# Optimization experiments

Hardware: AMD Instinct MI355X
Metric: run time of the kernel (lower is better)

The kernel has to match this reference:

```python
import jax, jax.numpy as jnp
import numpy as np

B, LQ, LK, DIM = 2, 2048, 2048, 1024
HEADS, DH = 8, 64
INNER = HEADS * DH  # 512


def setup_inputs() -> dict:
    key = jax.random.key(0)
    ks = jax.random.split(key, 7)
    x = jax.random.normal(ks[0], (B, LQ, DIM), dtype=jnp.float32)
    y = jax.random.normal(ks[1], (B, LK, DIM), dtype=jnp.float32)
    # binary mask, 1 => masked (gets -1e9 added)
    mask = jax.random.randint(ks[2], (B, LQ, LK), 0, 2).astype(jnp.float32)
    s = 0.02
    Wq = jax.random.normal(ks[3], (INNER, DIM), dtype=jnp.float32) * s
    Wk = jax.random.normal(ks[4], (INNER, DIM), dtype=jnp.float32) * s
    Wv = jax.random.normal(ks[5], (INNER, DIM), dtype=jnp.float32) * s
    Wo = jax.random.normal(ks[6], (DIM, INNER), dtype=jnp.float32) * s
    return {"x": x, "y": y, "mask": mask, "Wq": Wq, "Wk": Wk, "Wv": Wv, "Wo": Wo}


def reference(x, y, mask, Wq, Wk, Wv, Wo):
    scale = DH ** -0.5
    # projections (Linear without bias: x @ W.T)
    q = (x @ Wq.T) * scale            # [B, LQ, INNER]
    k = y @ Wk.T                      # [B, LK, INNER]
    v = y @ Wv.T                      # [B, LK, INNER]
    # split into heads (torch.split along last dim == reshape to [.., H, DH])
    q = q.reshape(B, LQ, HEADS, DH)
    k = k.reshape(B, LK, HEADS, DH)
    v = v.reshape(B, LK, HEADS, DH)
    # per-head QK^T + additive mask*-1e9, softmax over keys, then V
    scores = jnp.einsum('bqhd,bkhd->bhqk', q, k) + mask[:, None, :, :] * (-1e9)
    attn = jax.nn.softmax(scores, axis=-1)
    out = jnp.einsum('bhqk,bkhd->bqhd', attn, v).reshape(B, LQ, INNER)
    return out @ Wo.T                 # [B, LQ, DIM]
```

## Files before the change

### kernel.cpp

```cpp
#include <hip/hip_runtime.h>
#include <hip/hip_bf16.h>
#include <stdint.h>

#define BATCH 2
#define LQ 2048
#define LK 2048
#define DIM 1024
#define HEADS 8
#define DH 64
#define INNER 512

typedef __attribute__((ext_vector_type(8))) short short8;
typedef __attribute__((ext_vector_type(4))) float f32x4;

__device__ __forceinline__ float bf2f(unsigned short u) {
    union { unsigned int i; float f; } v;
    v.i = ((unsigned int)u) << 16;
    return v.f;
}
__device__ __forceinline__ unsigned short f2bf(float f) {
    __hip_bfloat16 h = __float2bfloat16(f);
    return *reinterpret_cast<unsigned short*>(&h);
}
__device__ __forceinline__ float fexp2(float x) {
#if __has_builtin(__builtin_amdgcn_exp2f)
    return __builtin_amdgcn_exp2f(x);
#else
    return __expf(x * 0.69314718056f);
#endif
}
__device__ __forceinline__ void stc(unsigned short* C, size_t i, float v) { C[i] = f2bf(v); }
__device__ __forceinline__ void stc(float* C, size_t i, float v) { C[i] = v; }

__device__ __forceinline__ unsigned cvtpk_bf16(float lo, float hi) {
    unsigned r;
    asm("v_cvt_pk_bf16_f32 %0, %1, %2" : "=v"(r) : "v"(lo), "v"(hi));
    return r;
}
__device__ __forceinline__ void perm32swap(unsigned& a, unsigned& b) {
#if __has_builtin(__builtin_amdgcn_permlane32_swap)
    auto r = __builtin_amdgcn_permlane32_swap(a, b, false, false);
    a = r[0]; b = r[1];
#else
    asm volatile("v_permlane32_swap_b32 %0, %1" : "+v"(a), "+v"(b));
#endif
}
__device__ __forceinline__ void perm16swap(unsigned& a, unsigned& b) {
#if __has_builtin(__builtin_amdgcn_permlane16_swap)
    auto r = __builtin_amdgcn_permlane16_swap(a, b, false, false);
    a = r[0]; b = r[1];
#else
    asm volatile("v_permlane16_swap_b32 %0, %1" : "+v"(a), "+v"(b));
#endif
}

typedef __attribute__((address_space(1))) const unsigned int gu32;
typedef __attribute__((address_space(3))) unsigned int lu32;
__device__ __forceinline__ void gload16(const void* g, void* l) {
    __builtin_amdgcn_global_load_lds((gu32*)g, (lu32*)l, 16, 0, 0);
}

__global__ __launch_bounds__(256) void prep(
    const float* __restrict__ x,  const float* __restrict__ y,
    const float* __restrict__ wq, const float* __restrict__ wk,
    const float* __restrict__ wv, const float* __restrict__ wo,
    const float* __restrict__ mask,
    unsigned short* __restrict__ xb,  unsigned short* __restrict__ yb,
    unsigned short* __restrict__ wqb, unsigned short* __restrict__ wkb,
    unsigned short* __restrict__ wvb, unsigned short* __restrict__ wob,
    unsigned long long* __restrict__ mbits)
{
    if (blockIdx.y == 6) {
        const int wid = blockIdx.x * 4 + (threadIdx.x >> 6);
        const int lane = threadIdx.x & 63;
        for (int task = wid; task < BATCH * LQ * 8; task += 4096) {
            int row = task >> 3, g = task & 7;
            const float* mp = mask + (size_t)row * LK + g * 256;
            unsigned long long* ob = mbits + (size_t)row * (LK / 64) + g * 4;
            float v0 = mp[0 * 64 + lane];
            float v1 = mp[1 * 64 + lane];
            float v2 = mp[2 * 64 + lane];
            float v3 = mp[3 * 64 + lane];
            unsigned long long b0 = __ballot(v0 > 0.5f);
            unsigned long long b1 = __ballot(v1 > 0.5f);
            unsigned long long b2 = __ballot(v2 > 0.5f);
            unsigned long long b3 = __ballot(v3 > 0.5f);
            if (lane == 0) { ob[0] = b0; ob[1] = b1; ob[2] = b2; ob[3] = b3; }
        }
        return;
    }
    const float* src; unsigned short* dst; int n4;
    switch (blockIdx.y) {
        case 0: src = x;  dst = xb;  n4 = (BATCH * LQ * DIM) / 4; break;
        case 1: src = y;  dst = yb;  n4 = (BATCH * LK * DIM) / 4; break;
        case 2: src = wq; dst = wqb; n4 = (INNER * DIM) / 4; break;
        case 3: src = wk; dst = wkb; n4 = (INNER * DIM) / 4; break;
        case 4: src = wv; dst = wvb; n4 = (INNER * DIM) / 4; break;
        default: src = wo; dst = wob; n4 = (INNER * DIM) / 4; break;
    }
    const int stride = gridDim.x * 256;
    for (int i = blockIdx.x * 256 + threadIdx.x; i < n4; i += stride) {
        float4 f = ((const float4*)src)[i];
        ushort4 u;
        u.x = f2bf(f.x); u.y = f2bf(f.y); u.z = f2bf(f.z); u.w = f2bf(f.w);
        ((ushort4*)dst)[i] = u;
    }
}

template <int IM, int JN, int WR, int WC, typename TC, int EPI>
__device__ __forceinline__ void gemm_body(
    const unsigned short* __restrict__ A,
    const unsigned short* __restrict__ W,
    TC* __restrict__ C,
    int K, int N, float scale,
    unsigned short* SH)
{
    constexpr int THREADS = WR * WC * 64;
    constexpr int BM = WR * IM * 16;
    constexpr int BN = WC * JN * 16;
    constexpr int ACH = BM * 8;
    constexpr int BCH = BN * 8;
    constexpr int AUS = BM * 64;
    constexpr int BUS = BN * 64;

    unsigned short* As = SH;
    unsigned short* Bs = SH + 2 * AUS;

    const int tid = threadIdx.x;
    const int m0 = blockIdx.x * BM;
    const int n0 = blockIdx.y * BN;
    const int w = tid >> 6, lane = tid & 63;
    const int q4 = lane >> 4, l16 = lane & 15;
    const int wm = (w / WC) * (IM * 16), wn = (w % WC) * (JN * 16);
    const int sw = l16 & 7;

    f32x4 acc[IM][JN] = {};

#pragma unroll
    for (int i = 0; i < ACH / THREADS; ++i) {
        int s = tid + i * THREADS;
        int r = s >> 3, ch = (s & 7) ^ (r & 7);
        gload16(A + (size_t)(m0 + r) * K + ch * 8, As + (size_t)s * 8);
    }
#pragma unroll
    for (int i = 0; i < BCH / THREADS; ++i) {
        int s = tid + i * THREADS;
        int r = s >> 3, ch = (s & 7) ^ (r & 7);
        gload16(W + (size_t)(n0 + r) * K + ch * 8, Bs + (size_t)s * 8);
    }
    __syncthreads();

    const int nt = K / 64;
    for (int t = 0; t < nt; ++t) {
        const int curA = (t & 1) * AUS;
        const int curB = (t & 1) * BUS;
        if (t + 1 < nt) {
            int kk = (t + 1) * 64;
            const int nxtA = AUS - curA, nxtB = BUS - curB;
#pragma unroll
            for (int i = 0; i < ACH / THREADS; ++i) {
                int s = tid + i * THREADS;
                int r = s >> 3, ch = (s & 7) ^ (r & 7);
                gload16(A + (size_t)(m0 + r) * K + kk + ch * 8, As + nxtA + (size_t)s * 8);
            }
#pragma unroll
            for (int i = 0; i < BCH / THREADS; ++i) {
                int s = tid + i * THREADS;
                int r = s >> 3, ch = (s & 7) ^ (r & 7);
                gload16(W + (size_t)(n0 + r) * K + kk + ch * 8, Bs + nxtB + (size_t)s * 8);
            }
        }

#pragma unroll
        for (int ks = 0; ks < 2; ++ks) {
            const int kq = ((ks * 4 + q4) ^ sw) * 8;
            short8 a[IM], b[JN];
#pragma unroll
            for (int i = 0; i < IM; ++i)
                a[i] = *(const short8*)(As + curA + (wm + i * 16 + l16) * 64 + kq);
#pragma unroll
            for (int j = 0; j < JN; ++j)
                b[j] = *(const short8*)(Bs + curB + (wn + j * 16 + l16) * 64 + kq);
#pragma unroll
            for (int i = 0; i < IM; ++i)
#pragma unroll
                for (int j = 0; j < JN; ++j)
                    acc[i][j] = __builtin_amdgcn_mfma_f32_16x16x32_bf16(
                        a[i], b[j], acc[i][j], 0, 0, 0);
        }
        __syncthreads();
    }

    if (EPI == 0) {
#pragma unroll
        for (int i = 0; i < IM; ++i)
#pragma unroll
            for (int j = 0; j < JN; ++j)
#pragma unroll
                for (int r = 0; r < 4; ++r) {
                    int row = m0 + wm + i * 16 + q4 * 4 + r;
                    int col = n0 + wn + j * 16 + l16;
                    stc(C, (size_t)row * N + col, acc[i][j][r] * scale);
                }
    } else {
        constexpr int KW = IM * 16;
        constexpr int DW = JN * 16;
        constexpr int TPS = KW + 8;
        unsigned short* TP = SH + w * (DW * TPS);
#pragma unroll
        for (int i = 0; i < IM; ++i)
#pragma unroll
            for (int j = 0; j < JN; ++j) {
                ushort4 u;
                u.x = f2bf(acc[i][j][0]); u.y = f2bf(acc[i][j][1]);
                u.z = f2bf(acc[i][j][2]); u.w = f2bf(acc[i][j][3]);
                *(ushort4*)(TP + (j * 16 + l16) * TPS + i * 16 + q4 * 4) = u;
            }
        const int keyflat = m0 + wm;
        const int bb = keyflat >> 11, key0 = keyflat & (LK - 1);
        const int hh = (n0 + wn) >> 6;
        const int dlow = (n0 + wn) & 63;
        constexpr int RCH = KW / 8;
        constexpr int NCH = DW * RCH;
#pragma unroll
        for (int p = 0; p < NCH / 64; ++p) {
            int c = p * 64 + lane;
            int dl = c / RCH, kc = c % RCH;
            uint4 v = *(const uint4*)(TP + dl * TPS + kc * 8);
            *(uint4*)((unsigned short*)C +
                ((size_t)((bb * HEADS + hh) * DH + dlow + dl)) * LK + key0 + kc * 8) = v;
        }
    }
}

#define QSCALE 0.18033688011112042f

__global__ __launch_bounds__(512) void proj_qkv(
    const unsigned short* __restrict__ xb, const unsigned short* __restrict__ yb,
    const unsigned short* __restrict__ wqb, const unsigned short* __restrict__ wkb,
    const unsigned short* __restrict__ wvb,
    unsigned short* __restrict__ qb, unsigned short* __restrict__ kb,
    unsigned short* __restrict__ vt)
{
    __shared__ __align__(16) unsigned short SH[4 * 128 * 64];
    const int z = blockIdx.z;
    const unsigned short* A = (z == 0) ? xb : yb;
    const unsigned short* W = (z == 0) ? wqb : (z == 1) ? wkb : wvb;
    if (z == 2)
        gemm_body<4, 2, 2, 4, unsigned short, 1>(A, W, vt, DIM, INNER, 1.0f, SH);
    else
        gemm_body<4, 2, 2, 4, unsigned short, 0>(A, W, (z == 0) ? qb : kb, DIM, INNER,
                                                 (z == 0) ? QSCALE : 1.0f, SH);
}

__global__ __launch_bounds__(512) void gemm_out(
    const unsigned short* __restrict__ A,
    const unsigned short* __restrict__ W,
    float* __restrict__ C)
{
    __shared__ __align__(16) unsigned short SH[4 * 128 * 64];
    gemm_body<4, 2, 2, 4, float, 0>(A, W, C, INNER, DIM, 1.0f, SH);
}

#define AT_SLOT (64 * 64)

__global__ __launch_bounds__(512, 4) void attn_mfma(
    const unsigned short* __restrict__ Q,
    const unsigned short* __restrict__ Kb,
    const unsigned short* __restrict__ Vt,
    const unsigned long long* __restrict__ Mb,
    unsigned short* __restrict__ O)
{
    __shared__ __align__(16) unsigned short Ks[4 * AT_SLOT];
    __shared__ __align__(16) unsigned short Vs[4 * AT_SLOT];

    const int tid = threadIdx.x;
    const int L = blockIdx.x;
    const int h = L & 7;
    const int jj = L >> 3;
    const int b = jj >> 5;
    const int q0 = (jj & 31) * 64;
    const int w = tid >> 6, lane = tid & 63;
    const int g = w & 3;
    const int par = w >> 2;
    const int q4 = lane >> 4, l16 = lane & 15;
    const int sw = l16 & 7;

    short8 qf[2];
    {
        const unsigned short* qp =
            Q + (size_t)(b * LQ + q0 + g * 16 + l16) * INNER + h * DH + q4 * 8;
        qf[0] = *(const short8*)(qp);
        qf[1] = *(const short8*)(qp + 32);
    }

    f32x4 o[4] = {};
    float lacc = 0.f;

    const unsigned short* kbase = Kb + (size_t)(b * LK) * INNER + h * DH;
    const unsigned short* vbase = Vt + (size_t)((b * HEADS + h) * DH) * LK;
    const unsigned long long* mrow =
        Mb + (size_t)(b * LQ + q0 + g * 16 + l16) * (LK / 64);

    const int rr = tid >> 3;
    const int ch = (tid & 7) ^ (rr & 7);

#pragma unroll
    for (int tn = 0; tn < 2; ++tn) {
        gload16(kbase + (size_t)(tn * 64 + rr) * INNER + ch * 8,
                Ks + tn * AT_SLOT + (size_t)tid * 8);
        gload16(vbase + (size_t)rr * LK + tn * 64 + ch * 8,
                Vs + tn * AT_SLOT + (size_t)tid * 8);
    }
    __syncthreads();

    const int NR = LK / 128;
    for (int rd = 0; rd < NR; ++rd) {
        if (rd + 1 < NR) {
#pragma unroll
            for (int i = 0; i < 2; ++i) {
                const int tn = 2 * rd + 2 + i;
                const int sl = tn & 3;
                gload16(kbase + (size_t)(tn * 64 + rr) * INNER + ch * 8,
                        Ks + sl * AT_SLOT + (size_t)tid * 8);
                gload16(vbase + (size_t)rr * LK + tn * 64 + ch * 8,
                        Vs + sl * AT_SLOT + (size_t)tid * 8);
            }
        }
        const int t = 2 * rd + par;
        const int cur = (t & 3) * AT_SLOT;

        f32x4 s[4];
        __builtin_amdgcn_s_setprio(1);
#pragma unroll
        for (int j = 0; j < 4; ++j) {
            s[j] = f32x4{0.f, 0.f, 0.f, 0.f};
#pragma unroll
            for (int ks = 0; ks < 2; ++ks) {
                short8 kf = *(const short8*)(Ks + cur + (j * 16 + l16) * 64
                                             + (((ks * 4 + q4) ^ sw) * 8));
                s[j] = __builtin_amdgcn_mfma_f32_16x16x32_bf16(kf, qf[ks], s[j], 0, 0, 0);
            }
        }
        __builtin_amdgcn_s_setprio(0);

        unsigned long long bsh = mrow[t] >> (q4 * 4);
        unsigned pk[8];
#pragma unroll
        for (int j = 0; j < 4; ++j) {
            unsigned nib = (unsigned)(bsh >> (16 * j)) & 0xFu;
            float p0 = (nib & 1u) ? 0.f : fexp2(s[j][0]);
            float p1 = (nib & 2u) ? 0.f : fexp2(s[j][1]);
            float p2 = (nib & 4u) ? 0.f : fexp2(s[j][2]);
            float p3 = (nib & 8u) ? 0.f : fexp2(s[j][3]);
            lacc += (p0 + p1) + (p2 + p3);
            pk[2 * j]     = cvtpk_bf16(p0, p1);
            pk[2 * j + 1] = cvtpk_bf16(p2, p3);
        }

        short8 pf[2];
#pragma unroll
        for (int ks = 0; ks < 2; ++ks) {
            unsigned a0 = pk[4 * ks + 0], b0 = pk[4 * ks + 2];
            unsigned a1 = pk[4 * ks + 1], b1 = pk[4 * ks + 3];
            perm32swap(a0, b0); perm16swap(a0, b0);
            perm32swap(a1, b1); perm16swap(a1, b1);
            union { unsigned u[4]; short8 s8; } up;
            up.u[0] = a0; up.u[1] = a1; up.u[2] = b0; up.u[3] = b1;
            pf[ks] = up.s8;
        }

        __builtin_amdgcn_s_setprio(1);
#pragma unroll
        for (int ks = 0; ks < 2; ++ks) {
#pragma unroll
            for (int dd = 0; dd < 4; ++dd) {
                short8 vf = *(const short8*)(Vs + cur + (dd * 16 + l16) * 64
                                             + (((ks * 4 + q4) ^ sw) * 8));
                o[dd] = __builtin_amdgcn_mfma_f32_16x16x32_bf16(vf, pf[ks], o[dd], 0, 0, 0);
            }
        }
        __builtin_amdgcn_s_setprio(0);
        __syncthreads();
    }

    float* xch = (float*)Ks;
    if (par) {
        float* d = xch + (size_t)(g * 64 + lane) * 17;
#pragma unroll
        for (int dd = 0; dd < 4; ++dd)
#pragma unroll
            for (int r2 = 0; r2 < 4; ++r2) d[dd * 4 + r2] = o[dd][r2];
        d[16] = lacc;
    }
    __syncthreads();
    if (!par) {
        const float* d = xch + (size_t)(g * 64 + lane) * 17;
#pragma unroll
        for (int dd = 0; dd < 4; ++dd)
#pragma unroll
            for (int r2 = 0; r2 < 4; ++r2) o[dd][r2] += d[dd * 4 + r2];
        lacc += d[16];

        lacc += __shfl_xor(lacc, 16);
        lacc += __shfl_xor(lacc, 32);
        const float inv = 1.0f / lacc;

        unsigned short* orow =
            O + (size_t)(b * LQ + q0 + g * 16 + l16) * INNER + h * DH + q4 * 4;
#pragma unroll
        for (int dd = 0; dd < 4; ++dd) {
            ushort4 u;
            u.x = f2bf(o[dd][0] * inv); u.y = f2bf(o[dd][1] * inv);
            u.z = f2bf(o[dd][2] * inv); u.w = f2bf(o[dd][3] * inv);
            *(ushort4*)(orow + dd * 16) = u;
        }
    }
}

extern "C" void kernel_launch(void* const* d_in, const int* in_sizes, int n_in,
                              void* d_out, int out_size, void* d_ws, size_t ws_size,
                              hipStream_t stream) {
    const float* x    = (const float*)d_in[0];
    const float* y    = (const float*)d_in[1];
    const float* mask = (const float*)d_in[2];
    const float* Wq   = (const float*)d_in[3];
    const float* Wk   = (const float*)d_in[4];
    const float* Wv   = (const float*)d_in[5];
    const float* Wo   = (const float*)d_in[6];
    float* out = (float*)d_out;

    const size_t NX = (size_t)BATCH * LQ * DIM;
    const size_t NS = (size_t)BATCH * LQ * INNER;
    const size_t NW = (size_t)INNER * DIM;
    unsigned short* xb  = (unsigned short*)d_ws;
    unsigned short* yb  = xb + NX;
    unsigned short* qb  = yb + NX;
    unsigned short* kb  = qb + NS;
    unsigned short* vt  = kb + NS;
    unsigned short* wqb = vt + NS;
    unsigned short* wkb = wqb + NW;
    unsigned short* wvb = wkb + NW;
    unsigned short* wob = wvb + NW;
    unsigned long long* mbits = (unsigned long long*)(wob + NW);
    unsigned short* ao  = xb;

    dim3 blk(256);
    prep<<<dim3(1024, 7), blk, 0, stream>>>(
        x, y, Wq, Wk, Wv, Wo, mask, xb, yb, wqb, wkb, wvb, wob, mbits);
    proj_qkv<<<dim3(4096 / 128, INNER / 128, 3), dim3(512), 0, stream>>>(
        xb, yb, wqb, wkb, wvb, qb, kb, vt);
    attn_mfma<<<dim3(512), dim3(512), 0, stream>>>(
        qb, kb, vt, mbits, ao);
    gemm_out<<<dim3(4096 / 128, DIM / 128), dim3(512), 0, stream>>>(ao, wob, out);
}
```

Baseline: 174.0 us.

## Switch attention kernel to 32x32x16 MFMA tiles with four-way wave reduction

Rewrites the attention inner loop to use 32x32x16 bf16 MFMA instructions instead of 16x16x32. Each wave now covers 32 query rows and half of a 64-key tile, which reduces the number of MFMA issues and LDS fragment loads per tile. The P-matrix repack needs only permlane32 swaps. In exchange, partial outputs are split four ways across waves and must be reduced through LDS at the end, and the larger accumulators raise register pressure.

```diff
diff --git a/kernel.cpp b/kernel.cpp
--- a/kernel.cpp
+++ b/kernel.cpp
@@ -12,6 +12,7 @@
 
 typedef __attribute__((ext_vector_type(8))) short short8;
 typedef __attribute__((ext_vector_type(4))) float f32x4;
+typedef __attribute__((ext_vector_type(16))) float f32x16;
 
 __device__ __forceinline__ float bf2f(unsigned short u) {
     union { unsigned int i; float f; } v;
@@ -43,14 +44,6 @@
     a = r[0]; b = r[1];
 #else
     asm volatile("v_permlane32_swap_b32 %0, %1" : "+v"(a), "+v"(b));
-#endif
-}
-__device__ __forceinline__ void perm16swap(unsigned& a, unsigned& b) {
-#if __has_builtin(__builtin_amdgcn_permlane16_swap)
-    auto r = __builtin_amdgcn_permlane16_swap(a, b, false, false);
-    a = r[0]; b = r[1];
-#else
-    asm volatile("v_permlane16_swap_b32 %0, %1" : "+v"(a), "+v"(b));
 #endif
 }
 
@@ -281,26 +274,27 @@
     const int b = jj >> 5;
     const int q0 = (jj & 31) * 64;
     const int w = tid >> 6, lane = tid & 63;
-    const int g = w & 3;
+    const int qh = w & 1;
+    const int kh = (w >> 1) & 1;
     const int par = w >> 2;
-    const int q4 = lane >> 4, l16 = lane & 15;
-    const int sw = l16 & 7;
-
-    short8 qf[2];
+    const int l31 = lane & 31, hl = lane >> 5;
+
+    short8 qf[4];
     {
         const unsigned short* qp =
-            Q + (size_t)(b * LQ + q0 + g * 16 + l16) * INNER + h * DH + q4 * 8;
-        qf[0] = *(const short8*)(qp);
-        qf[1] = *(const short8*)(qp + 32);
-    }
-
-    f32x4 o[4] = {};
+            Q + (size_t)(b * LQ + q0 + qh * 32 + l31) * INNER + h * DH + 8 * hl;
+#pragma unroll
+        for (int ks = 0; ks < 4; ++ks)
+            qf[ks] = *(const short8*)(qp + ks * 16);
+    }
+
+    f32x16 o[2] = {};
     float lacc = 0.f;
 
     const unsigned short* kbase = Kb + (size_t)(b * LK) * INNER + h * DH;
     const unsigned short* vbase = Vt + (size_t)((b * HEADS + h) * DH) * LK;
     const unsigned long long* mrow =
-        Mb + (size_t)(b * LQ + q0 + g * 16 + l16) * (LK / 64);
+        Mb + (size_t)(b * LQ + q0 + qh * 32 + l31) * (LK / 64);
 
     const int rr = tid >> 3;
     const int ch = (tid & 7) ^ (rr & 7);
@@ -314,6 +308,7 @@
     }
     __syncthreads();
 
+    const int l7 = lane & 7;
     const int NR = LK / 128;
     for (int rd = 0; rd < NR; ++rd) {
         if (rd + 1 < NR) {
@@ -330,91 +325,95 @@
         const int t = 2 * rd + par;
         const int cur = (t & 3) * AT_SLOT;
 
-        f32x4 s[4];
+        f32x16 s = {};
         __builtin_amdgcn_s_setprio(1);
 #pragma unroll
-        for (int j = 0; j < 4; ++j) {
-            s[j] = f32x4{0.f, 0.f, 0.f, 0.f};
-#pragma unroll
-            for (int ks = 0; ks < 2; ++ks) {
-                short8 kf = *(const short8*)(Ks + cur + (j * 16 + l16) * 64
-                                             + (((ks * 4 + q4) ^ sw) * 8));
-                s[j] = __builtin_amdgcn_mfma_f32_16x16x32_bf16(kf, qf[ks], s[j], 0, 0, 0);
-            }
+        for (int ks = 0; ks < 4; ++ks) {
+            const int R = kh * 32 + l31;
+            const int c0 = ks * 2 + hl;
+            short8 kf = *(const short8*)(Ks + cur + R * 64 + ((c0 ^ l7) * 8));
+            s = __builtin_amdgcn_mfma_f32_32x32x16_bf16(kf, qf[ks], s, 0, 0, 0);
         }
         __builtin_amdgcn_s_setprio(0);
 
-        unsigned long long bsh = mrow[t] >> (q4 * 4);
+        unsigned bits32 = (unsigned)(mrow[t] >> (kh * 32));
         unsigned pk[8];
 #pragma unroll
-        for (int j = 0; j < 4; ++j) {
-            unsigned nib = (unsigned)(bsh >> (16 * j)) & 0xFu;
-            float p0 = (nib & 1u) ? 0.f : fexp2(s[j][0]);
-            float p1 = (nib & 2u) ? 0.f : fexp2(s[j][1]);
-            float p2 = (nib & 4u) ? 0.f : fexp2(s[j][2]);
-            float p3 = (nib & 8u) ? 0.f : fexp2(s[j][3]);
+        for (int g = 0; g < 4; ++g) {
+            unsigned nib = (bits32 >> (8 * g + 4 * hl)) & 0xFu;
+            float p0 = (nib & 1u) ? 0.f : fexp2(s[4 * g + 0]);
+            float p1 = (nib & 2u) ? 0.f : fexp2(s[4 * g + 1]);
+            float p2 = (nib & 4u) ? 0.f : fexp2(s[4 * g + 2]);
+            float p3 = (nib & 8u) ? 0.f : fexp2(s[4 * g + 3]);
             lacc += (p0 + p1) + (p2 + p3);
-            pk[2 * j]     = cvtpk_bf16(p0, p1);
-            pk[2 * j + 1] = cvtpk_bf16(p2, p3);
+            pk[2 * g]     = cvtpk_bf16(p0, p1);
+            pk[2 * g + 1] = cvtpk_bf16(p2, p3);
         }
 
         short8 pf[2];
 #pragma unroll
-        for (int ks = 0; ks < 2; ++ks) {
-            unsigned a0 = pk[4 * ks + 0], b0 = pk[4 * ks + 2];
-            unsigned a1 = pk[4 * ks + 1], b1 = pk[4 * ks + 3];
-            perm32swap(a0, b0); perm16swap(a0, b0);
-            perm32swap(a1, b1); perm16swap(a1, b1);
+        for (int k2 = 0; k2 < 2; ++k2) {
+            unsigned r0 = pk[4 * k2 + 0], r2 = pk[4 * k2 + 2];
+            unsigned r1 = pk[4 * k2 + 1], r3 = pk[4 * k2 + 3];
+            perm32swap(r0, r2);
+            perm32swap(r1, r3);
             union { unsigned u[4]; short8 s8; } up;
-            up.u[0] = a0; up.u[1] = a1; up.u[2] = b0; up.u[3] = b1;
-            pf[ks] = up.s8;
+            up.u[0] = r0; up.u[1] = r1; up.u[2] = r2; up.u[3] = r3;
+            pf[k2] = up.s8;
         }
 
         __builtin_amdgcn_s_setprio(1);
 #pragma unroll
-        for (int ks = 0; ks < 2; ++ks) {
-#pragma unroll
-            for (int dd = 0; dd < 4; ++dd) {
-                short8 vf = *(const short8*)(Vs + cur + (dd * 16 + l16) * 64
-                                             + (((ks * 4 + q4) ^ sw) * 8));
-                o[dd] = __builtin_amdgcn_mfma_f32_16x16x32_bf16(vf, pf[ks], o[dd], 0, 0, 0);
+        for (int df = 0; df < 2; ++df) {
+#pragma unroll
+            for (int k2 = 0; k2 < 2; ++k2) {
+                const int R = df * 32 + l31;
+                const int c0 = kh * 4 + k2 * 2 + hl;
+                short8 vf = *(const short8*)(Vs + cur + R * 64 + ((c0 ^ l7) * 8));
+                o[df] = __builtin_amdgcn_mfma_f32_32x32x16_bf16(vf, pf[k2], o[df], 0, 0, 0);
             }
         }
         __builtin_amdgcn_s_setprio(0);
         __syncthreads();
     }
 
-    float* xch = (float*)Ks;
-    if (par) {
-        float* d = xch + (size_t)(g * 64 + lane) * 17;
-#pragma unroll
-        for (int dd = 0; dd < 4; ++dd)
-#pragma unroll
-            for (int r2 = 0; r2 < 4; ++r2) d[dd * 4 + r2] = o[dd][r2];
-        d[16] = lacc;
+    float* xq = (float*)(qh ? (void*)Vs : (void*)Ks);
+    const int wslot = par * 2 + kh;
+    if (wslot) {
+        float* d = xq + (size_t)((wslot - 1) * 64 + lane) * 33;
+#pragma unroll
+        for (int df = 0; df < 2; ++df)
+#pragma unroll
+            for (int r = 0; r < 16; ++r) d[df * 16 + r] = o[df][r];
+        d[32] = lacc;
     }
     __syncthreads();
-    if (!par) {
-        const float* d = xch + (size_t)(g * 64 + lane) * 17;
-#pragma unroll
-        for (int dd = 0; dd < 4; ++dd)
-#pragma unroll
-            for (int r2 = 0; r2 < 4; ++r2) o[dd][r2] += d[dd * 4 + r2];
-        lacc += d[16];
-
-        lacc += __shfl_xor(lacc, 16);
+    if (!wslot) {
+#pragma unroll
+        for (int ws2 = 0; ws2 < 3; ++ws2) {
+            const float* d = xq + (size_t)(ws2 * 64 + lane) * 33;
+#pragma unroll
+            for (int df = 0; df < 2; ++df)
+#pragma unroll
+                for (int r = 0; r < 16; ++r) o[df][r] += d[df * 16 + r];
+            lacc += d[32];
+        }
         lacc += __shfl_xor(lacc, 32);
         const float inv = 1.0f / lacc;
 
         unsigned short* orow =
-            O + (size_t)(b * LQ + q0 + g * 16 + l16) * INNER + h * DH + q4 * 4;
-#pragma unroll
-        for (int dd = 0; dd < 4; ++dd) {
-            ushort4 u;
-            u.x = f2bf(o[dd][0] * inv); u.y = f2bf(o[dd][1] * inv);
-            u.z = f2bf(o[dd][2] * inv); u.w = f2bf(o[dd][3] * inv);
-            *(ushort4*)(orow + dd * 16) = u;
-        }
+            O + (size_t)(b * LQ + q0 + qh * 32 + l31) * INNER + h * DH;
+#pragma unroll
+        for (int df = 0; df < 2; ++df)
+#pragma unroll
+            for (int g = 0; g < 4; ++g) {
+                ushort4 u;
+                u.x = f2bf(o[df][4 * g + 0] * inv);
+                u.y = f2bf(o[df][4 * g + 1] * inv);
+                u.z = f2bf(o[df][4 * g + 2] * inv);
+                u.w = f2bf(o[df][4 * g + 3] * inv);
+                *(ushort4*)(orow + df * 32 + 8 * g + 4 * hl) = u;
+            }
     }
 }
 
```

Result: no change. 174.0 us (-0.0%).
